# Kernel optimization log

Measured on AMD Instinct MI355X. Metric: run time of the kernel, lower is better.

## Reference

```python
import jax, jax.numpy as jnp
import numpy as np

COUPLING = 1.0
DT = 1.0
ATTRACTION = 1.0
EPS = 1e-6


def setup_inputs() -> dict:
    key = jax.random.key(0)
    k1, k2, k3, k4 = jax.random.split(key, 4)
    B, N, D = 4, 2048, 4
    theta_prev = jax.random.normal(k1, (B, N, D), dtype=jnp.float32)
    gamma_prev = jax.random.normal(k2, (B, N, D), dtype=jnp.float32)
    theta_connectivity_weight = jax.random.uniform(k3, (B, N, N), dtype=jnp.float32)
    alpha_t = jax.random.normal(k4, (B, N, N), dtype=jnp.float32)
    return {
        "theta_prev": theta_prev,
        "gamma_prev": gamma_prev,
        "theta_connectivity_weight": theta_connectivity_weight,
        "alpha_t": alpha_t,
    }


def reference(theta_prev, gamma_prev, theta_connectivity_weight, alpha_t):
    # Pairwise coupling: coupling/N * sum_j W[b,i,j] * sin(theta[b,j,d] - theta[b,i,d] - alpha[b,i,j])
    # Expanded via trig identities so the O(N^2*D) tensor is never materialized:
    #   sin(tj - ti - a) = cos(a)*(s_j c_i - c_j s_i) - sin(a)*(c_j c_i + s_j s_i)
    # => sum_j W_ij sin(...) = c_i*(A s)_i - s_i*(A c)_i - c_i*(Bm c)_i - s_i*(Bm s)_i
    # with A = W*cos(alpha), Bm = W*sin(alpha). This matches the chunked torch loop exactly.
    n = theta_prev.shape[1]
    s = jnp.sin(theta_prev)  # [B, N, D]
    c = jnp.cos(theta_prev)  # [B, N, D]
    A = theta_connectivity_weight * jnp.cos(alpha_t)   # [B, N, N]
    Bm = theta_connectivity_weight * jnp.sin(alpha_t)  # [B, N, N]
    As = jnp.einsum("bij,bjd->bid", A, s)
    Ac = jnp.einsum("bij,bjd->bid", A, c)
    Bs = jnp.einsum("bij,bjd->bid", Bm, s)
    Bc = jnp.einsum("bij,bjd->bid", Bm, c)
    coupling_term = (COUPLING / n) * (c * As - s * Ac - c * Bc - s * Bs)
    drive_term = ATTRACTION * (gamma_prev - theta_prev)
    theta_next = theta_prev + DT * (drive_term + coupling_term)
    # torch F.normalize: x / clamp(||x||_2, min=eps) along last dim
    norm = jnp.linalg.norm(theta_next, axis=-1, keepdims=True)
    return theta_next / jnp.maximum(norm, EPS)
```

## Files before the change

kernel.cpp:

```cpp
#include <hip/hip_runtime.h>
#include <stdint.h>

#define N_NODES 2048
#define N_BATCH 4
#define ROWS_PER_BLOCK 8
#define THREADS 512

__device__ __forceinline__ uint32_t bf16rn(float x) {
    uint32_t u = __float_as_uint(x);
    u += 0x7fffu + ((u >> 16) & 1u);
    return u >> 16;
}

__global__ __launch_bounds__(THREADS, 8) void kuramoto_kernel(
    const float* __restrict__ theta,
    const float* __restrict__ gamma,
    const float* __restrict__ W,
    const float* __restrict__ alpha,
    float* __restrict__ out)
{
    __shared__ uint4 table[N_NODES];

    const int tid  = threadIdx.x;
    const int lane = tid & 63;
    const int wave = tid >> 6;
    const int b    = blockIdx.x >> 8;
    const int i    = ((blockIdx.x & 255) * ROWS_PER_BLOCK) + wave;

    const float* thb = theta + (size_t)b * (N_NODES * 4);
    #pragma unroll
    for (int g = 0; g < N_NODES / THREADS; ++g) {
        const int j = tid + g * THREADS;
        const float4 u = *(const float4*)(thb + (size_t)j * 4);
        const float th[4] = {u.x, u.y, u.z, u.w};
        uint32_t p[4];
        #pragma unroll
        for (int d = 0; d < 4; ++d) {
            float s, c;
            __sincosf(th[d], &s, &c);
            p[d] = (bf16rn(c) << 16) | bf16rn(s);
        }
        table[j] = make_uint4(p[0], p[1], p[2], p[3]);
    }
    __syncthreads();

    const size_t rowbase = ((size_t)b * N_NODES + i) * N_NODES;
    const float* Wr = W + rowbase;
    const float* Ar = alpha + rowbase;

    float re[4] = {0.f, 0.f, 0.f, 0.f};
    float im[4] = {0.f, 0.f, 0.f, 0.f};

    #pragma unroll 8
    for (int it = 0; it < N_NODES / 64; ++it) {
        const int j = it * 64 + lane;
        const float w = Wr[j];
        const float a = Ar[j];
        float sa, ca;
        __sincosf(a, &sa, &ca);
        const float A  = w * ca;
        const float Bq = w * sa;
        const uint4 t = table[j];
        const uint32_t tw[4] = {t.x, t.y, t.z, t.w};
        #pragma unroll
        for (int d = 0; d < 4; ++d) {
            const float s = __uint_as_float(tw[d] << 16);
            const float c = __uint_as_float(tw[d] & 0xffff0000u);
            re[d] = fmaf(A,  c, re[d]);
            re[d] = fmaf(Bq, s, re[d]);
            im[d] = fmaf(A,  s, im[d]);
            im[d] = fmaf(-Bq, c, im[d]);
        }
    }

    #pragma unroll
    for (int stage = 1; stage < 64; stage <<= 1) {
        #pragma unroll
        for (int d = 0; d < 4; ++d) {
            re[d] += __shfl_xor(re[d], stage, 64);
            im[d] += __shfl_xor(im[d], stage, 64);
        }
    }

    if (lane == 0) {
        const size_t obase = ((size_t)b * N_NODES + i) * 4;
        const float4 th4 = *(const float4*)(thb + (size_t)i * 4);
        const float4 g4  = *(const float4*)(gamma + obase);
        const float thd[4] = {th4.x, th4.y, th4.z, th4.w};
        const float gd[4]  = {g4.x, g4.y, g4.z, g4.w};
        float t[4];
        float s2 = 0.0f;
        #pragma unroll
        for (int d = 0; d < 4; ++d) {
            float s_i, c_i;
            __sincosf(thd[d], &s_i, &c_i);
            const float coup = (c_i * im[d] - s_i * re[d]) * (1.0f / (float)N_NODES);
            t[d] = gd[d] + coup;
            s2 = fmaf(t[d], t[d], s2);
        }
        const float inv = 1.0f / fmaxf(sqrtf(s2), 1e-6f);
        *(float4*)(out + obase) = make_float4(t[0]*inv, t[1]*inv, t[2]*inv, t[3]*inv);
    }
}

extern "C" void kernel_launch(void* const* d_in, const int* in_sizes, int n_in,
                              void* d_out, int out_size, void* d_ws, size_t ws_size,
                              hipStream_t stream) {
    const float* theta = (const float*)d_in[0];
    const float* gamma = (const float*)d_in[1];
    const float* W     = (const float*)d_in[2];
    const float* alpha = (const float*)d_in[3];
    float* out = (float*)d_out;

    const int grid = (N_BATCH * N_NODES) / ROWS_PER_BLOCK;
    hipLaunchKernelGGL(kuramoto_kernel, dim3(grid), dim3(THREADS), 0, stream,
                       theta, gamma, W, alpha, out);
}
```

Baseline: 152.4 us.

## Vectorize W/alpha loads to float4 with software prefetch and transpose sincos table

After: 152.8 us. Within noise of the previous version (+0.3%).

```diff
diff --git a/kernel.cpp b/kernel.cpp
--- a/kernel.cpp
+++ b/kernel.cpp
@@ -12,14 +12,14 @@
     return u >> 16;
 }
 
-__global__ __launch_bounds__(THREADS, 8) void kuramoto_kernel(
+__global__ __launch_bounds__(THREADS, 4) void kuramoto_kernel(
     const float* __restrict__ theta,
     const float* __restrict__ gamma,
     const float* __restrict__ W,
     const float* __restrict__ alpha,
     float* __restrict__ out)
 {
-    __shared__ uint4 table[N_NODES];
+    __shared__ uint32_t scTab[4][N_NODES];
 
     const int tid  = threadIdx.x;
     const int lane = tid & 63;
@@ -33,14 +33,12 @@
         const int j = tid + g * THREADS;
         const float4 u = *(const float4*)(thb + (size_t)j * 4);
         const float th[4] = {u.x, u.y, u.z, u.w};
-        uint32_t p[4];
         #pragma unroll
         for (int d = 0; d < 4; ++d) {
             float s, c;
             __sincosf(th[d], &s, &c);
-            p[d] = (bf16rn(c) << 16) | bf16rn(s);
+            scTab[d][j] = (bf16rn(c) << 16) | bf16rn(s);
         }
-        table[j] = make_uint4(p[0], p[1], p[2], p[3]);
     }
     __syncthreads();
 
@@ -51,26 +49,44 @@
     float re[4] = {0.f, 0.f, 0.f, 0.f};
     float im[4] = {0.f, 0.f, 0.f, 0.f};
 
-    #pragma unroll 8
-    for (int it = 0; it < N_NODES / 64; ++it) {
-        const int j = it * 64 + lane;
-        const float w = Wr[j];
-        const float a = Ar[j];
-        float sa, ca;
-        __sincosf(a, &sa, &ca);
-        const float A  = w * ca;
-        const float Bq = w * sa;
-        const uint4 t = table[j];
-        const uint32_t tw[4] = {t.x, t.y, t.z, t.w};
+    float4 w4 = *(const float4*)(Wr + 4 * lane);
+    float4 a4 = *(const float4*)(Ar + 4 * lane);
+
+    #pragma unroll
+    for (int it = 0; it < N_NODES / 256; ++it) {
+        float4 w4n, a4n;
+        if (it < N_NODES / 256 - 1) {
+            const int nb = (it + 1) * 256 + 4 * lane;
+            w4n = *(const float4*)(Wr + nb);
+            a4n = *(const float4*)(Ar + nb);
+        }
+        const int jb = it * 256 + 4 * lane;
+        const float wk[4] = {w4.x, w4.y, w4.z, w4.w};
+        const float ak[4] = {a4.x, a4.y, a4.z, a4.w};
+        float A[4], Bq[4];
+        #pragma unroll
+        for (int k = 0; k < 4; ++k) {
+            float sa, ca;
+            __sincosf(ak[k], &sa, &ca);
+            A[k]  = wk[k] * ca;
+            Bq[k] = wk[k] * sa;
+        }
         #pragma unroll
         for (int d = 0; d < 4; ++d) {
-            const float s = __uint_as_float(tw[d] << 16);
-            const float c = __uint_as_float(tw[d] & 0xffff0000u);
-            re[d] = fmaf(A,  c, re[d]);
-            re[d] = fmaf(Bq, s, re[d]);
-            im[d] = fmaf(A,  s, im[d]);
-            im[d] = fmaf(-Bq, c, im[d]);
+            const uint4 t = *(const uint4*)(&scTab[d][jb]);
+            const uint32_t tw[4] = {t.x, t.y, t.z, t.w};
+            #pragma unroll
+            for (int k = 0; k < 4; ++k) {
+                const float s = __uint_as_float(tw[k] << 16);
+                const float c = __uint_as_float(tw[k] & 0xffff0000u);
+                re[d] = fmaf(A[k],  c, re[d]);
+                re[d] = fmaf(Bq[k], s, re[d]);
+                im[d] = fmaf(A[k],  s, im[d]);
+                im[d] = fmaf(-Bq[k], c, im[d]);
+            }
         }
+        w4 = w4n;
+        a4 = a4n;
     }
 
     #pragma unroll
```
